# Optimization experiments

Hardware: AMD Instinct MI355X
Metric: run time of the kernel (lower is better)

Reference implementation:

```python
import jax, jax.numpy as jnp
import numpy as np

N = 150000      # nodes
E_AST = 300000  # ast edges
E_CFG = 250000  # cfg edges
D = 256         # in_size = out_size
N_STEPS = 2


def _gru(a, h, Wih, Whh, bih, bhh):
    # torch.nn.GRUCell semantics: input a, hidden h
    gi = a @ Wih.T + bih            # [N, 3D]
    gh = h @ Whh.T + bhh            # [N, 3D]
    ir, iz, i_n = jnp.split(gi, 3, axis=-1)
    hr, hz, h_n = jnp.split(gh, 3, axis=-1)
    r = jax.nn.sigmoid(ir + hr)
    z = jax.nn.sigmoid(iz + hz)
    n = jnp.tanh(i_n + r * h_n)
    return (1.0 - z) * n + z * h


def _gated_graph_conv(h, src, dst, W, b, Wih, Whh, bih, bhh):
    # DGL GatedGraphConv, n_etypes=1, in_feats == out_feats
    n_nodes = h.shape[0]
    for _ in range(N_STEPS):
        m = (h @ W.T + b)[src]                                   # per-edge gather [E, D]
        a = jax.ops.segment_sum(m, dst, num_segments=n_nodes)    # scatter-sum to dst
        h = _gru(a, h, Wih, Whh, bih, bhh)
    return h


def setup_inputs() -> dict:
    key = jax.random.key(0)
    ks = jax.random.split(key, 16)
    s = 1.0 / np.sqrt(D)
    inp = {
        'nodes': jax.random.normal(ks[0], (N, D), jnp.float32),
        'ast_src': jax.random.randint(ks[1], (E_AST,), 0, N),
        'ast_dst': jax.random.randint(ks[2], (E_AST,), 0, N),
        'cfg_src': jax.random.randint(ks[3], (E_CFG,), 0, N),
        'cfg_dst': jax.random.randint(ks[4], (E_CFG,), 0, N),
        'W_ast': jax.random.normal(ks[5], (D, D), jnp.float32) * s,
        'b_ast': jnp.zeros((D,), jnp.float32),
        'Wih_ast': jax.random.normal(ks[6], (3 * D, D), jnp.float32) * s,
        'Whh_ast': jax.random.normal(ks[7], (3 * D, D), jnp.float32) * s,
        'bih_ast': jnp.zeros((3 * D,), jnp.float32),
        'bhh_ast': jnp.zeros((3 * D,), jnp.float32),
        'w1': jax.random.normal(ks[8], (D, 2 * D), jnp.float32) * (1.0 / np.sqrt(2 * D)),
        'b1': jnp.zeros((D,), jnp.float32),
        'W_cpg': jax.random.normal(ks[9], (D, D), jnp.float32) * s,
        'b_cpg': jnp.zeros((D,), jnp.float32),
        'Wih_cpg': jax.random.normal(ks[10], (3 * D, D), jnp.float32) * s,
        'Whh_cpg': jax.random.normal(ks[11], (3 * D, D), jnp.float32) * s,
        'bih_cpg': jnp.zeros((3 * D,), jnp.float32),
        'bhh_cpg': jnp.zeros((3 * D,), jnp.float32),
        'w2': jax.random.normal(ks[12], (D, 2 * D), jnp.float32) * (1.0 / np.sqrt(2 * D)),
        'b2': jnp.zeros((D,), jnp.float32),
    }
    return inp


def reference(nodes, ast_src, ast_dst, cfg_src, cfg_dst,
              W_ast, b_ast, Wih_ast, Whh_ast, bih_ast, bhh_ast,
              w1, b1,
              W_cpg, b_cpg, Wih_cpg, Whh_cpg, bih_cpg, bhh_cpg,
              w2, b2):
    # ast branch: GatedGraphConv -> concat with input -> fn_1
    h_ast = _gated_graph_conv(nodes, ast_src, ast_dst,
                              W_ast, b_ast, Wih_ast, Whh_ast, bih_ast, bhh_ast)
    hiddens = jnp.concatenate([h_ast, nodes], axis=-1) @ w1.T + b1   # [N, D]
    # cpg branch: GatedGraphConv -> concat with hiddens -> fn_2
    h_cpg = _gated_graph_conv(hiddens, cfg_src, cfg_dst,
                              W_cpg, b_cpg, Wih_cpg, Whh_cpg, bih_cpg, bhh_cpg)
    logits = jnp.concatenate([h_cpg, hiddens], axis=-1) @ w2.T + b2  # [N, D]
    return logits
```

## Files before the change

kernel.cpp:

```cpp
#include <hip/hip_runtime.h>

typedef _Float16 f16;
typedef _Float16 f16x8 __attribute__((ext_vector_type(8)));
typedef float f32x16 __attribute__((ext_vector_type(16)));

__device__ __forceinline__ f16x8 zero8() {
  f16x8 v;
#pragma unroll
  for (int j = 0; j < 8; ++j) v[j] = (f16)0.f;
  return v;
}

__device__ __forceinline__ f16x8 cvt8p(const float* p) {
  float4 a = *(const float4*)p;
  float4 b = *(const float4*)(p + 4);
  f16x8 v;
  v[0] = (f16)a.x; v[1] = (f16)a.y; v[2] = (f16)a.z; v[3] = (f16)a.w;
  v[4] = (f16)b.x; v[5] = (f16)b.y; v[6] = (f16)b.z; v[7] = (f16)b.w;
  return v;
}

__device__ __forceinline__ void gload16(const void* g, void* l) {
  __builtin_amdgcn_global_load_lds((const __attribute__((address_space(1))) unsigned int*)g,
                                   (__attribute__((address_space(3))) unsigned int*)l, 16, 0, 0);
}

__device__ __forceinline__ float sigm(float x) {
  return __builtin_amdgcn_rcpf(1.f + __expf(-x));
}
__device__ __forceinline__ float tanh_(float x) {
  x = fminf(15.f, fmaxf(-15.f, x));
  float e = __expf(2.f * x);
  return 1.f - 2.f * __builtin_amdgcn_rcpf(e + 1.f);
}


__global__ void k_cvt8(const float* __restrict__ x, f16* __restrict__ y, long n) {
  long i = ((long)blockIdx.x * blockDim.x + threadIdx.x) * 8;
  long stride = (long)gridDim.x * blockDim.x * 8;
  for (; i < n; i += stride) *(f16x8*)(y + i) = cvt8p(x + i);
}

__global__ void k_wc2(const float* __restrict__ Wih, const float* __restrict__ W,
                      unsigned char* __restrict__ dstb) {
  int j = blockIdx.x;
  int k = threadIdx.x;
  float s = 0.f;
  for (int c = 0; c < 256; ++c) s = fmaf(Wih[j * 256 + c], W[c * 256 + k], s);
  int g = j >> 8, hcol = j & 255;
  int hb = hcol >> 5, trow = hcol & 31;
  int kc = k >> 6, kl = k & 63;
  int slot = (kl >> 3) ^ (trow & 7);
  size_t byte = (size_t)hb * 98304 + (size_t)kc * 12288 +
                (size_t)(g * 32 + trow) * 128 + slot * 16 + (kl & 7) * 2;
  *(f16*)(dstb + byte) = (f16)s;
}

__global__ void k_whh2(const float* __restrict__ Whh, unsigned char* __restrict__ dstb) {
  int j = blockIdx.x;
  int k = threadIdx.x;
  float s = Whh[j * 256 + k];
  int g = j >> 8, hcol = j & 255;
  int hb = hcol >> 5, trow = hcol & 31;
  int kc = 4 + (k >> 6), kl = k & 63;
  int slot = (kl >> 3) ^ (trow & 7);
  size_t byte = (size_t)hb * 98304 + (size_t)kc * 12288 +
                (size_t)(g * 32 + trow) * 128 + slot * 16 + (kl & 7) * 2;
  *(f16*)(dstb + byte) = (f16)s;
}

__global__ void k_prepw(const float* __restrict__ w, unsigned char* __restrict__ dstb) {
  int j = blockIdx.x;
  for (int k = threadIdx.x; k < 512; k += 256) {
    int chunk = k >> 7, kl = k & 127;
    int slot = ((kl >> 3) + ((j >> 3) & 3)) & 15;
    size_t byte = (size_t)chunk * 69632 + (size_t)j * 272 + slot * 16 + (kl & 7) * 2;
    *(f16*)(dstb + byte) = (f16)w[j * 512 + k];
  }
}

__global__ void k_v(const float* __restrict__ Wih, const float* __restrict__ b,
                    float* __restrict__ v) {
  int j = blockIdx.x * blockDim.x + threadIdx.x;
  if (j < 768) {
    float s = 0.f;
    for (int c = 0; c < 256; ++c) s = fmaf(Wih[j * 256 + c], b[c], s);
    v[j] = s;
  }
}

__global__ void k_hist(const int* __restrict__ dst, int* __restrict__ cnt, int E) {
  int e = blockIdx.x * 256 + threadIdx.x;
  if (e < E) atomicAdd(&cnt[dst[e]], 1);
}

__global__ void k_scan1(const int* __restrict__ deg, int* __restrict__ rowptr,
                        int* __restrict__ bsum, int n) {
  __shared__ int buf[256];
  int i = blockIdx.x * 256 + threadIdx.x;
  int v = (i < n) ? deg[i] : 0;
  buf[threadIdx.x] = v;
  __syncthreads();
  for (int off = 1; off < 256; off <<= 1) {
    int t = 0;
    if ((int)threadIdx.x >= off) t = buf[threadIdx.x - off];
    __syncthreads();
    buf[threadIdx.x] += t;
    __syncthreads();
  }
  if (i < n) rowptr[i] = buf[threadIdx.x] - v;
  if (threadIdx.x == 255) bsum[blockIdx.x] = buf[255];
}

__global__ void k_scan2(int* __restrict__ bsum, int nb) {
  __shared__ int buf[1024];
  int v = ((int)threadIdx.x < nb) ? bsum[threadIdx.x] : 0;
  buf[threadIdx.x] = v;
  __syncthreads();
  for (int off = 1; off < 1024; off <<= 1) {
    int t = 0;
    if ((int)threadIdx.x >= off) t = buf[threadIdx.x - off];
    __syncthreads();
    buf[threadIdx.x] += t;
    __syncthreads();
  }
  if ((int)threadIdx.x < nb) bsum[threadIdx.x] = buf[threadIdx.x] - v;
}

__global__ void k_scan3(int* __restrict__ rowptr, const int* __restrict__ bsum,
                        int n, int E) {
  int i = blockIdx.x * 256 + threadIdx.x;
  if (i < n) rowptr[i] += bsum[blockIdx.x];
  if (i == n) rowptr[n] = E;
}

__global__ void k_fill(const int* __restrict__ src, const int* __restrict__ dst,
                       const int* __restrict__ rowptr, int* __restrict__ cnt,
                       int* __restrict__ esrc, int E) {
  int e = blockIdx.x * 256 + threadIdx.x;
  if (e < E) {
    int d = dst[e];
    int r = atomicAdd(&cnt[d], 1);
    esrc[rowptr[d] + r] = src[e];
  }
}

__global__ void k_gather(const f16* __restrict__ h, const int* __restrict__ rowptr,
                         const int* __restrict__ esrc, f16* __restrict__ ag, int n) {
  int g = threadIdx.x >> 5, l = threadIdx.x & 31;
  int node = blockIdx.x * 8 + g;
  if (node >= n) return;
  int e0 = rowptr[node], e1 = rowptr[node + 1];
  float acc[8];
#pragma unroll
  for (int j = 0; j < 8; ++j) acc[j] = 0.f;
  for (int e = e0; e < e1; ++e) {
    int s = esrc[e];
    f16x8 hv = *(const f16x8*)(h + (long)s * 256 + l * 8);
#pragma unroll
    for (int j = 0; j < 8; ++j) acc[j] += (float)hv[j];
  }
  f16x8 o;
#pragma unroll
  for (int j = 0; j < 8; ++j) o[j] = (f16)acc[j];
  *(f16x8*)(ag + (long)node * 256 + l * 8) = o;
}

__global__ __launch_bounds__(256, 4) void k_gru(
    const f16* __restrict__ ag, const f16* __restrict__ hin,
    const unsigned char* __restrict__ wprep, const float* __restrict__ bih,
    const float* __restrict__ bhh, const float* __restrict__ vv,
    const int* __restrict__ rowptr, f16* __restrict__ hout, int n, int nper) {
  __shared__ unsigned char SM[24576 + 512];
  float* Ds = (float*)(SM + 24576);
  int bid = blockIdx.x;
  int w = (bid & 7) * nper + (bid >> 3);
  int rt = w >> 3, hb = w & 7;
  int row0 = rt * 128;
  int tid = threadIdx.x, lane = tid & 63, wid = tid >> 6;
  int l31 = lane & 31, hi = lane >> 5;
  const unsigned char* wb = wprep + (size_t)hb * 98304;

  auto stage = [&](int c, unsigned char* dst) {
    const unsigned char* s0 = wb + (size_t)c * 12288;
#pragma unroll
    for (int i = 0; i < 3; ++i) {
      int r = i * 4 + wid;
      gload16(s0 + r * 1024 + lane * 16, dst + r * 1024);
    }
  };

  int arow = row0 + wid * 32 + l31;
  bool aok = arow < n;
  const f16* agp = ag + (size_t)arow * 256 + hi * 8;
  const f16* hp = hin + (size_t)arow * 256 + hi * 8;

  f16x8 a[4];
  auto loadA = [&](const f16* p, int koff) {
#pragma unroll
    for (int ks = 0; ks < 4; ++ks)
      a[ks] = aok ? *(const f16x8*)(p + koff + ks * 16) : zero8();
  };
  int sl0 = l31 & 7;
  auto runC = [&](const unsigned char* Bb, f32x16& aR, f32x16& aZ, f32x16& aN) {
#pragma unroll
    for (int ks = 0; ks < 4; ++ks) {
      int sl = (ks * 2 + hi) ^ sl0;
      const unsigned char* base = Bb + sl * 16;
      f16x8 b0 = *(const f16x8*)(base + (0 * 32 + l31) * 128);
      aR = __builtin_amdgcn_mfma_f32_32x32x16_f16(a[ks], b0, aR, 0, 0, 0);
      f16x8 b1 = *(const f16x8*)(base + (1 * 32 + l31) * 128);
      aZ = __builtin_amdgcn_mfma_f32_32x32x16_f16(a[ks], b1, aZ, 0, 0, 0);
      f16x8 b2 = *(const f16x8*)(base + (2 * 32 + l31) * 128);
      aN = __builtin_amdgcn_mfma_f32_32x32x16_f16(a[ks], b2, aN, 0, 0, 0);
    }
  };

  f32x16 accR, accZ, accNI, accNH;
#pragma unroll
  for (int j = 0; j < 16; ++j) { accR[j] = 0.f; accZ[j] = 0.f; accNI[j] = 0.f; accNH[j] = 0.f; }

  stage(0, SM);
  loadA(agp, 0);
  if (tid < 128) {
    int grow = row0 + tid;
    Ds[tid] = (grow < n) ? (float)(rowptr[grow + 1] - rowptr[grow]) : 0.f;
  }
  __syncthreads();

  stage(1, SM + 12288);
  runC(SM, accR, accZ, accNI);
  loadA(agp, 64);
  __syncthreads();
  stage(2, SM);
  runC(SM + 12288, accR, accZ, accNI);
  loadA(agp, 128);
  __syncthreads();
  stage(3, SM + 12288);
  runC(SM, accR, accZ, accNI);
  loadA(agp, 192);
  __syncthreads();
  stage(4, SM);
  runC(SM + 12288, accR, accZ, accNI);
  loadA(hp, 0);
  __syncthreads();
  stage(5, SM + 12288);
  runC(SM, accR, accZ, accNH);
  loadA(hp, 64);
  __syncthreads();
  stage(6, SM);
  runC(SM + 12288, accR, accZ, accNH);
  loadA(hp, 128);
  __syncthreads();
  stage(7, SM + 12288);
  runC(SM, accR, accZ, accNH);
  loadA(hp, 192);
  __syncthreads();
  runC(SM + 12288, accR, accZ, accNH);

  int gcol = hb * 32 + l31;
  float br = bih[gcol] + bhh[gcol];
  float bz = bih[256 + gcol] + bhh[256 + gcol];
  float bi_n = bih[512 + gcol], bh_n = bhh[512 + gcol];
  float vr = vv[gcol], vz = vv[256 + gcol], vn = vv[512 + gcol];
  int wrow = wid * 32;

#pragma unroll
  for (int rg = 0; rg < 16; ++rg) {
    int crow = (rg & 3) + 8 * (rg >> 2) + 4 * hi;
    int grow = row0 + wrow + crow;
    float dg = Ds[wrow + crow];
    float hold = (grow < n) ? (float)hin[(size_t)grow * 256 + gcol] : 0.f;
    float r = sigm(accR[rg] + br + dg * vr);
    float z = sigm(accZ[rg] + bz + dg * vz);
    float nn = tanh_(accNI[rg] + bi_n + dg * vn + r * (accNH[rg] + bh_n));
    if (grow < n)
      hout[(size_t)grow * 256 + gcol] = (f16)((1.f - z) * nn + z * hold);
  }
}

__global__ __launch_bounds__(512, 2) void k_fn(
    const f16* __restrict__ hb, const float* __restrict__ base,
    const unsigned char* __restrict__ wp, const float* __restrict__ bias,
    float* __restrict__ out, int n) {
  __shared__ unsigned char SM[69632];
  int row0 = blockIdx.x * 128;
  int tid = threadIdx.x, lane = tid & 63, wid = tid >> 6;
  int l31 = lane & 31, hi = lane >> 5;
  int rs = wid >> 2, cgf = wid & 3;
  int arow[2];
  arow[0] = row0 + rs * 64 + l31;
  arow[1] = arow[0] + 32;
  int srot = (l31 >> 3) & 3;

  f32x16 acc[2][2];
#pragma unroll
  for (int q = 0; q < 2; ++q)
#pragma unroll
    for (int t = 0; t < 2; ++t)
#pragma unroll
      for (int j = 0; j < 16; ++j) acc[q][t][j] = 0.f;

#pragma unroll
  for (int c = 0; c < 4; ++c) {
    if (c) __syncthreads();
    for (int i = wid; i < 68; i += 8)
      gload16(wp + (size_t)c * 69632 + i * 1024 + lane * 16, SM + i * 1024);
    f16x8 areg[2][8];
#pragma unroll
    for (int q = 0; q < 2; ++q) {
      bool ok = arow[q] < n;
#pragma unroll
      for (int ks = 0; ks < 8; ++ks) {
        int k = c * 128 + ks * 16 + hi * 8;
        if (!ok)
          areg[q][ks] = zero8();
        else if (k < 256)
          areg[q][ks] = *(const f16x8*)(hb + (size_t)arow[q] * 256 + k);
        else
          areg[q][ks] = cvt8p(base + (size_t)arow[q] * 256 + (k - 256));
      }
    }
    __syncthreads();
#pragma unroll
    for (int ks = 0; ks < 8; ++ks) {
      int slot = ((ks * 2 + hi) + srot) & 15;
#pragma unroll
      for (int t = 0; t < 2; ++t) {
        int R = cgf * 64 + t * 32 + l31;
        f16x8 b = *(const f16x8*)(SM + R * 272 + slot * 16);
        acc[0][t] = __builtin_amdgcn_mfma_f32_32x32x16_f16(areg[0][ks], b, acc[0][t], 0, 0, 0);
        acc[1][t] = __builtin_amdgcn_mfma_f32_32x32x16_f16(areg[1][ks], b, acc[1][t], 0, 0, 0);
      }
    }
  }

#pragma unroll
  for (int t = 0; t < 2; ++t) {
    int col = cgf * 64 + t * 32 + l31;
    float bb = bias[col];
#pragma unroll
    for (int q = 0; q < 2; ++q) {
#pragma unroll
      for (int rg = 0; rg < 16; ++rg) {
        int grow = row0 + rs * 64 + q * 32 + (rg & 3) + 8 * (rg >> 2) + 4 * hi;
        if (grow < n) out[(size_t)grow * 256 + col] = acc[q][t][rg] + bb;
      }
    }
  }
}

extern "C" void kernel_launch(void* const* d_in, const int* in_sizes, int n_in,
                              void* d_out, int out_size, void* d_ws, size_t ws_size,
                              hipStream_t stream) {
  const float* nodes = (const float*)d_in[0];
  const int* asrc = (const int*)d_in[1];
  const int* adst = (const int*)d_in[2];
  const int* csrc = (const int*)d_in[3];
  const int* cdst = (const int*)d_in[4];
  const float* W_ast = (const float*)d_in[5];
  const float* b_ast = (const float*)d_in[6];
  const float* Wih_a = (const float*)d_in[7];
  const float* Whh_a = (const float*)d_in[8];
  const float* bih_a = (const float*)d_in[9];
  const float* bhh_a = (const float*)d_in[10];
  const float* w1 = (const float*)d_in[11];
  const float* b1 = (const float*)d_in[12];
  const float* W_cpg = (const float*)d_in[13];
  const float* b_cpg = (const float*)d_in[14];
  const float* Wih_c = (const float*)d_in[15];
  const float* Whh_c = (const float*)d_in[16];
  const float* bih_c = (const float*)d_in[17];
  const float* bhh_c = (const float*)d_in[18];
  const float* w2 = (const float*)d_in[19];
  const float* b2 = (const float*)d_in[20];
  float* out = (float*)d_out;

  const int N = in_sizes[0] / 256;
  const int EA = in_sizes[1];
  const int EC = in_sizes[3];
  const long ND = (long)N * 256;

  char* ws = (char*)d_ws;
  size_t off = 0;
  auto carve = [&](size_t bytes) -> char* {
    char* p = ws + off;
    off += (bytes + 255) & ~(size_t)255;
    return p;
  };
  f16* h0 = (f16*)carve(ND * 2);
  f16* h1 = (f16*)carve(ND * 2);
  f16* ag = (f16*)carve(ND * 2);
  unsigned char* wpA = (unsigned char*)carve(786432);
  unsigned char* wpC = (unsigned char*)carve(786432);
  unsigned char* w1p = (unsigned char*)carve(278528);
  unsigned char* w2p = (unsigned char*)carve(278528);
  float* vA = (float*)carve(768 * 4);
  float* vC = (float*)carve(768 * 4);
  int* rowptr = (int*)carve((size_t)(N + 1) * 4);
  int* cnt = (int*)carve((size_t)N * 4);
  int* esrc = (int*)carve((size_t)(EA > EC ? EA : EC) * 4);
  int* bsum = (int*)carve(1024 * 4);
  (void)ws_size; (void)n_in; (void)out_size;

  const int NRB = (N + 127) / 128;
  const int FBLK = (N + 127) / 128;
  const int SBLK = (N + 255) / 256;
  auto cvt = [&](const float* x, f16* y, long n) {
    int blocks = (int)((n / 8 + 255) / 256);
    if (blocks > 2048) blocks = 2048;
    k_cvt8<<<blocks, 256, 0, stream>>>(x, y, n);
  };

  k_wc2<<<768, 256, 0, stream>>>(Wih_a, W_ast, wpA);
  k_wc2<<<768, 256, 0, stream>>>(Wih_c, W_cpg, wpC);
  k_whh2<<<768, 256, 0, stream>>>(Whh_a, wpA);
  k_whh2<<<768, 256, 0, stream>>>(Whh_c, wpC);
  k_prepw<<<256, 256, 0, stream>>>(w1, w1p);
  k_prepw<<<256, 256, 0, stream>>>(w2, w2p);
  k_v<<<3, 256, 0, stream>>>(Wih_a, b_ast, vA);
  k_v<<<3, 256, 0, stream>>>(Wih_c, b_cpg, vC);
  cvt(nodes, h0, ND);

  auto run_branch = [&](const int* src, const int* dst, int E, const unsigned char* wprep,
                        const float* bih, const float* bhh, const float* v) {
    hipMemsetAsync(cnt, 0, (size_t)N * 4, stream);
    k_hist<<<(E + 255) / 256, 256, 0, stream>>>(dst, cnt, E);
    k_scan1<<<SBLK, 256, 0, stream>>>(cnt, rowptr, bsum, N);
    k_scan2<<<1, 1024, 0, stream>>>(bsum, SBLK);
    k_scan3<<<SBLK, 256, 0, stream>>>(rowptr, bsum, N, E);
    hipMemsetAsync(cnt, 0, (size_t)N * 4, stream);
    k_fill<<<(E + 255) / 256, 256, 0, stream>>>(src, dst, rowptr, cnt, esrc, E);
    k_gather<<<(N + 7) / 8, 256, 0, stream>>>(h0, rowptr, esrc, ag, N);
    k_gru<<<NRB * 8, 256, 0, stream>>>(ag, h0, wprep, bih, bhh, v, rowptr, h1, N, NRB);
    k_gather<<<(N + 7) / 8, 256, 0, stream>>>(h1, rowptr, esrc, ag, N);
    k_gru<<<NRB * 8, 256, 0, stream>>>(ag, h1, wprep, bih, bhh, v, rowptr, h0, N, NRB);
  };

  run_branch(asrc, adst, EA, wpA, bih_a, bhh_a, vA);
  k_fn<<<FBLK, 512, 0, stream>>>(h0, nodes, w1p, b1, out, N);
  cvt(out, h0, ND);
  run_branch(csrc, cdst, EC, wpC, bih_c, bhh_c, vC);
  k_fn<<<FBLK, 512, 0, stream>>>(h0, out, w2p, b2, out, N);
}
```

Measured before the change: 1.558 ms.

## Restructure output projection with double-buffered LDS tiles and f16 base inputs

Rewrites the final projection kernel so each block handles a 128x64 output tile. Weight chunks of 64 K are staged into two LDS buffers that alternate, so the next load overlaps the current MFMA work. The concat base input is now read as pre-converted f16 (a separate nd16 buffer) instead of converting fp32 inside the kernel, and the weight prep layout is changed to an XOR-swizzled 128-byte row format to match. The neighbor gather loop is also unrolled by two to keep two row loads in flight. The block remapping assumes the grid divides evenly by 8, and the change adds an extra N×256 f16 workspace buffer.

```diff
diff --git a/kernel.cpp b/kernel.cpp
--- a/kernel.cpp
+++ b/kernel.cpp
@@ -71,10 +71,11 @@
 
 __global__ void k_prepw(const float* __restrict__ w, unsigned char* __restrict__ dstb) {
   int j = blockIdx.x;
+  int cg = j >> 6, R = j & 63;
   for (int k = threadIdx.x; k < 512; k += 256) {
-    int chunk = k >> 7, kl = k & 127;
-    int slot = ((kl >> 3) + ((j >> 3) & 3)) & 15;
-    size_t byte = (size_t)chunk * 69632 + (size_t)j * 272 + slot * 16 + (kl & 7) * 2;
+    int kc = k >> 6, kl = k & 63;
+    int slot = (kl >> 3) ^ (R & 7);
+    size_t byte = (size_t)(cg * 8 + kc) * 8192 + (size_t)R * 128 + slot * 16 + (kl & 7) * 2;
     *(f16*)(dstb + byte) = (f16)w[j * 512 + k];
   }
 }
@@ -154,11 +155,19 @@
   float acc[8];
 #pragma unroll
   for (int j = 0; j < 8; ++j) acc[j] = 0.f;
-  for (int e = e0; e < e1; ++e) {
-    int s = esrc[e];
-    f16x8 hv = *(const f16x8*)(h + (long)s * 256 + l * 8);
-#pragma unroll
-    for (int j = 0; j < 8; ++j) acc[j] += (float)hv[j];
+  int e = e0;
+  for (; e + 2 <= e1; e += 2) {
+    int s0 = esrc[e], s1 = esrc[e + 1];
+    f16x8 hv0 = *(const f16x8*)(h + (long)s0 * 256 + l * 8);
+    f16x8 hv1 = *(const f16x8*)(h + (long)s1 * 256 + l * 8);
+#pragma unroll
+    for (int j = 0; j < 8; ++j) acc[j] += (float)hv0[j] + (float)hv1[j];
+  }
+  if (e < e1) {
+    int s0 = esrc[e];
+    f16x8 hv0 = *(const f16x8*)(h + (long)s0 * 256 + l * 8);
+#pragma unroll
+    for (int j = 0; j < 8; ++j) acc[j] += (float)hv0[j];
   }
   f16x8 o;
 #pragma unroll
@@ -279,73 +288,77 @@
   }
 }
 
-__global__ __launch_bounds__(512, 2) void k_fn(
-    const f16* __restrict__ hb, const float* __restrict__ base,
+__global__ __launch_bounds__(256, 4) void k_fn(
+    const f16* __restrict__ hb, const f16* __restrict__ base16,
     const unsigned char* __restrict__ wp, const float* __restrict__ bias,
-    float* __restrict__ out, int n) {
-  __shared__ unsigned char SM[69632];
-  int row0 = blockIdx.x * 128;
+    float* __restrict__ out, int n, int nper) {
+  __shared__ unsigned char SM[16384];
+  int bid = blockIdx.x;
+  int w = (bid & 7) * nper + (bid >> 3);
+  int rt = w >> 2, cg = w & 3;
+  int row0 = rt * 128;
   int tid = threadIdx.x, lane = tid & 63, wid = tid >> 6;
   int l31 = lane & 31, hi = lane >> 5;
-  int rs = wid >> 2, cgf = wid & 3;
-  int arow[2];
-  arow[0] = row0 + rs * 64 + l31;
-  arow[1] = arow[0] + 32;
-  int srot = (l31 >> 3) & 3;
-
-  f32x16 acc[2][2];
-#pragma unroll
-  for (int q = 0; q < 2; ++q)
-#pragma unroll
-    for (int t = 0; t < 2; ++t)
-#pragma unroll
-      for (int j = 0; j < 16; ++j) acc[q][t][j] = 0.f;
-
-#pragma unroll
-  for (int c = 0; c < 4; ++c) {
-    if (c) __syncthreads();
-    for (int i = wid; i < 68; i += 8)
-      gload16(wp + (size_t)c * 69632 + i * 1024 + lane * 16, SM + i * 1024);
-    f16x8 areg[2][8];
-#pragma unroll
-    for (int q = 0; q < 2; ++q) {
-      bool ok = arow[q] < n;
-#pragma unroll
-      for (int ks = 0; ks < 8; ++ks) {
-        int k = c * 128 + ks * 16 + hi * 8;
-        if (!ok)
-          areg[q][ks] = zero8();
-        else if (k < 256)
-          areg[q][ks] = *(const f16x8*)(hb + (size_t)arow[q] * 256 + k);
-        else
-          areg[q][ks] = cvt8p(base + (size_t)arow[q] * 256 + (k - 256));
-      }
+  const unsigned char* wb = wp + (size_t)cg * 65536;
+
+  auto stage = [&](int c, unsigned char* dst) {
+    const unsigned char* s0 = wb + (size_t)c * 8192;
+#pragma unroll
+    for (int i = 0; i < 2; ++i) {
+      int r = i * 4 + wid;
+      gload16(s0 + r * 1024 + lane * 16, dst + r * 1024);
     }
-    __syncthreads();
-#pragma unroll
-    for (int ks = 0; ks < 8; ++ks) {
-      int slot = ((ks * 2 + hi) + srot) & 15;
-#pragma unroll
-      for (int t = 0; t < 2; ++t) {
-        int R = cgf * 64 + t * 32 + l31;
-        f16x8 b = *(const f16x8*)(SM + R * 272 + slot * 16);
-        acc[0][t] = __builtin_amdgcn_mfma_f32_32x32x16_f16(areg[0][ks], b, acc[0][t], 0, 0, 0);
-        acc[1][t] = __builtin_amdgcn_mfma_f32_32x32x16_f16(areg[1][ks], b, acc[1][t], 0, 0, 0);
-      }
+  };
+
+  int arow = row0 + wid * 32 + l31;
+  bool aok = arow < n;
+  const f16* hbp = hb + (size_t)arow * 256 + hi * 8;
+  const f16* bsp = base16 + (size_t)arow * 256 + hi * 8;
+
+  f16x8 a[4];
+  auto loadA = [&](const f16* p, int koff) {
+#pragma unroll
+    for (int ks = 0; ks < 4; ++ks)
+      a[ks] = aok ? *(const f16x8*)(p + koff + ks * 16) : zero8();
+  };
+  int sl0 = l31 & 7;
+
+  f32x16 acc0, acc1;
+#pragma unroll
+  for (int j = 0; j < 16; ++j) { acc0[j] = 0.f; acc1[j] = 0.f; }
+
+  auto runC = [&](const unsigned char* Bb) {
+#pragma unroll
+    for (int ks = 0; ks < 4; ++ks) {
+      int sl = (ks * 2 + hi) ^ sl0;
+      const unsigned char* base = Bb + sl * 16;
+      f16x8 b0 = *(const f16x8*)(base + (0 + l31) * 128);
+      acc0 = __builtin_amdgcn_mfma_f32_32x32x16_f16(a[ks], b0, acc0, 0, 0, 0);
+      f16x8 b1 = *(const f16x8*)(base + (32 + l31) * 128);
+      acc1 = __builtin_amdgcn_mfma_f32_32x32x16_f16(a[ks], b1, acc1, 0, 0, 0);
     }
-  }
-
-#pragma unroll
-  for (int t = 0; t < 2; ++t) {
-    int col = cgf * 64 + t * 32 + l31;
-    float bb = bias[col];
-#pragma unroll
-    for (int q = 0; q < 2; ++q) {
-#pragma unroll
-      for (int rg = 0; rg < 16; ++rg) {
-        int grow = row0 + rs * 64 + q * 32 + (rg & 3) + 8 * (rg >> 2) + 4 * hi;
-        if (grow < n) out[(size_t)grow * 256 + col] = acc[q][t][rg] + bb;
-      }
+  };
+
+  stage(0, SM);
+  loadA(hbp, 0);
+  __syncthreads();
+  stage(1, SM + 8192); runC(SM);        loadA(hbp, 64);  __syncthreads();
+  stage(2, SM);        runC(SM + 8192); loadA(hbp, 128); __syncthreads();
+  stage(3, SM + 8192); runC(SM);        loadA(hbp, 192); __syncthreads();
+  stage(4, SM);        runC(SM + 8192); loadA(bsp, 0);   __syncthreads();
+  stage(5, SM + 8192); runC(SM);        loadA(bsp, 64);  __syncthreads();
+  stage(6, SM);        runC(SM + 8192); loadA(bsp, 128); __syncthreads();
+  stage(7, SM + 8192); runC(SM);        loadA(bsp, 192); __syncthreads();
+  runC(SM + 8192);
+
+  int colb = cg * 64;
+  float bb0 = bias[colb + l31], bb1 = bias[colb + 32 + l31];
+#pragma unroll
+  for (int rg = 0; rg < 16; ++rg) {
+    int grow = row0 + wid * 32 + (rg & 3) + 8 * (rg >> 2) + 4 * hi;
+    if (grow < n) {
+      out[(size_t)grow * 256 + colb + l31] = acc0[rg] + bb0;
+      out[(size_t)grow * 256 + colb + 32 + l31] = acc1[rg] + bb1;
     }
   }
 }
@@ -391,10 +404,11 @@
   f16* h0 = (f16*)carve(ND * 2);
   f16* h1 = (f16*)carve(ND * 2);
   f16* ag = (f16*)carve(ND * 2);
+  f16* nd16 = (f16*)carve(ND * 2);
   unsigned char* wpA = (unsigned char*)carve(786432);
   unsigned char* wpC = (unsigned char*)carve(786432);
-  unsigned char* w1p = (unsigned char*)carve(278528);
-  unsigned char* w2p = (unsigned char*)carve(278528);
+  unsigned char* w1p = (unsigned char*)carve(262144);
+  unsigned char* w2p = (unsigned char*)carve(262144);
   float* vA = (float*)carve(768 * 4);
   float* vC = (float*)carve(768 * 4);
   int* rowptr = (int*)carve((size_t)(N + 1) * 4);
@@ -404,7 +418,8 @@
   (void)ws_size; (void)n_in; (void)out_size;
 
   const int NRB = (N + 127) / 128;
-  const int FBLK = (N + 127) / 128;
+  const int GGRID = NRB * 8;
+  const int FGRID = NRB * 4;
   const int SBLK = (N + 255) / 256;
   auto cvt = [&](const float* x, f16* y, long n) {
     int blocks = (int)((n / 8 + 255) / 256);
@@ -420,10 +435,11 @@
   k_prepw<<<256, 256, 0, stream>>>(w2, w2p);
   k_v<<<3, 256, 0, stream>>>(Wih_a, b_ast, vA);
   k_v<<<3, 256, 0, stream>>>(Wih_c, b_cpg, vC);
-  cvt(nodes, h0, ND);
+  cvt(nodes, nd16, ND);
 
   auto run_branch = [&](const int* src, const int* dst, int E, const unsigned char* wprep,
-                        const float* bih, const float* bhh, const float* v) {
+                        const float* bih, const float* bhh, const float* v,
+                        const f16* hstart) {
     hipMemsetAsync(cnt, 0, (size_t)N * 4, stream);
     k_hist<<<(E + 255) / 256, 256, 0, stream>>>(dst, cnt, E);
     k_scan1<<<SBLK, 256, 0, stream>>>(cnt, rowptr, bsum, N);
@@ -431,15 +447,15 @@
     k_scan3<<<SBLK, 256, 0, stream>>>(rowptr, bsum, N, E);
     hipMemsetAsync(cnt, 0, (size_t)N * 4, stream);
     k_fill<<<(E + 255) / 256, 256, 0, stream>>>(src, dst, rowptr, cnt, esrc, E);
-    k_gather<<<(N + 7) / 8, 256, 0, stream>>>(h0, rowptr, esrc, ag, N);
-    k_gru<<<NRB * 8, 256, 0, stream>>>(ag, h0, wprep, bih, bhh, v, rowptr, h1, N, NRB);
+    k_gather<<<(N + 7) / 8, 256, 0, stream>>>(hstart, rowptr, esrc, ag, N);
+    k_gru<<<GGRID, 256, 0, stream>>>(ag, hstart, wprep, bih, bhh, v, rowptr, h1, N, NRB);
     k_gather<<<(N + 7) / 8, 256, 0, stream>>>(h1, rowptr, esrc, ag, N);
-    k_gru<<<NRB * 8, 256, 0, stream>>>(ag, h1, wprep, bih, bhh, v, rowptr, h0, N, NRB);
-  };
-
-  run_branch(asrc, adst, EA, wpA, bih_a, bhh_a, vA);
-  k_fn<<<FBLK, 512, 0, stream>>>(h0, nodes, w1p, b1, out, N);
-  cvt(out, h0, ND);
-  run_branch(csrc, cdst, EC, wpC, bih_c, bhh_c, vC);
-  k_fn<<<FBLK, 512, 0, stream>>>(h0, out, w2p, b2, out, N);
-}
+    k_gru<<<GGRID, 256, 0, stream>>>(ag, h1, wprep, bih, bhh, v, rowptr, h0, N, NRB);
+  };
+
+  run_branch(asrc, adst, EA, wpA, bih_a, bhh_a, vA, nd16);
+  k_fn<<<FGRID, 256, 0, stream>>>(h0, nd16, w1p, b1, out, N, NRB * 4 / 8);
+  cvt(out, nd16, ND);
+  run_branch(csrc, cdst, EC, wpC, bih_c, bhh_c, vC, nd16);
+  k_fn<<<FGRID, 256, 0, stream>>>(h0, nd16, w2p, b2, out, N, NRB * 4 / 8);
+}
```

Measured after the change: 1.384 ms. 11.1% less time.
